# Performance work log

Hardware: AMD Instinct MI355X
Metric: run time of the kernel (lower is better)

## Reference

```python
import jax, jax.numpy as jnp
import numpy as np

B, H, S, D = 1, 16, 4096, 64
TEMPERATURE = 8.0          # sqrt(d_k)
WINDOW_SIZE = 256
HALF_WINDOW = WINDOW_SIZE // 2
NEG_INF = -1000000000.0


def setup_inputs() -> dict:
    key = jax.random.key(0)
    kq, kk, kv = jax.random.split(key, 3)
    q = jax.random.normal(kq, (B, H, S, D), dtype=jnp.float32)
    k = jax.random.normal(kk, (B, H, S, D), dtype=jnp.float32)
    v = jax.random.normal(kv, (B, H, S, D), dtype=jnp.float32)
    return {"q": q, "k": k, "v": v}


def reference(q, k, v):
    # q,k,v: [B,H,S,D]
    seq = q.shape[2]
    attn = jnp.einsum('bhqd,bhkd->bhqk', q, k) / TEMPERATURE  # [B,H,S,S]
    if seq > WINDOW_SIZE:
        idx = jnp.arange(seq)
        # torch loop: row i allows columns [i-half, i+half] inclusive
        win = jnp.abs(idx[:, None] - idx[None, :]) <= HALF_WINDOW  # [S,S]
        attn = jnp.where(win[None, None, :, :], attn, NEG_INF)
    attn = jax.nn.softmax(attn, axis=-1)  # dropout p=0 -> identity
    out = jnp.einsum('bhqk,bhkd->bhqd', attn, v)
    return (out, attn)
```

## Files before the change

kernel.cpp:

```cpp
#include <hip/hip_runtime.h>
#include <hip/hip_bf16.h>


typedef short bf16x8 __attribute__((ext_vector_type(8)));
typedef float f32x4  __attribute__((ext_vector_type(4)));
typedef unsigned int u32;
typedef unsigned short u16;

namespace {
constexpr int S = 4096, H = 16, Dh = 64, TR = 16, HW = 128, NCH = 5;
constexpr int UW  = NCH * 64;
constexpr int KP  = 72;
constexpr int PBW = UW + 8;
}

__device__ __forceinline__ u16 f2bf(float x) {
    u32 u = __float_as_uint(x);
    return (u16)((u + 0x7fffu + ((u >> 16) & 1u)) >> 16);
}
__device__ __forceinline__ float bf2f(u16 h) {
    return __uint_as_float(((u32)h) << 16);
}

__global__ __launch_bounds__(256, 4)
void wattn(const float* __restrict__ q, const float* __restrict__ k,
           const float* __restrict__ v, float* __restrict__ out,
           float* __restrict__ attn)
{
    __shared__ __align__(16) u16 hbuf[16768];
    __shared__ float red[TR * 4];
    __shared__ float inv_row[TR];
    u16* qh_ = hbuf;
    u16* ql_ = hbuf + 1152;
    u16* kh_ = hbuf + 2304;
    u16* kl_ = hbuf + 6912;
    u16* pb_ = hbuf + 11520;

    const int tid  = threadIdx.x;
    const int wave = tid >> 6, lane = tid & 63;
    const int g = lane >> 4, m = lane & 15;

    int bx = blockIdx.x;
    bx = (bx & 7) * (H * (S / TR) / 8) + (bx >> 3);
    const int h  = bx >> 8;
    const int r0 = (bx & 255) * TR;
    const int c0 = max(0, r0 - HW);
    const int c1 = min(S - 1, r0 + TR - 1 + HW);

    const float* qp = q + ((size_t)h * S + r0) * Dh;
    const float* kp = k + (size_t)h * S * Dh;
    const float* vp = v + (size_t)h * S * Dh;

    {
        const int row = tid >> 4, d4 = (tid & 15) * 4;
        float4 t = *(const float4*)(qp + row * Dh + d4);
        float xs[4] = {t.x, t.y, t.z, t.w};
        u16* dh = qh_ + row * KP + d4;
        u16* dl = ql_ + row * KP + d4;
        #pragma unroll
        for (int i = 0; i < 4; ++i) {
            u16 hi = f2bf(xs[i]);
            dh[i] = hi;
            dl[i] = f2bf(xs[i] - bf2f(hi));
        }
    }
    __syncthreads();

    bf16x8 aqh[2], aql[2];
    #pragma unroll
    for (int ks = 0; ks < 2; ++ks) {
        aqh[ks] = *(const bf16x8*)(qh_ + m * KP + ks * 32 + g * 8);
        aql[ks] = *(const bf16x8*)(ql_ + m * KP + ks * 32 + g * 8);
    }

    f32x4 sc[NCH];
    #pragma unroll
    for (int cc = 0; cc < NCH; ++cc) {
        const int col = tid >> 2, d16 = (tid & 3) * 16;
        const int cg  = min(c0 + cc * 64 + col, S - 1);
        const float* src = kp + (size_t)cg * Dh + d16;
        u16* dh = kh_ + col * KP + d16;
        u16* dl = kl_ + col * KP + d16;
        #pragma unroll
        for (int i4 = 0; i4 < 4; ++i4) {
            float4 t = *(const float4*)(src + i4 * 4);
            float xs[4] = {t.x, t.y, t.z, t.w};
            #pragma unroll
            for (int i = 0; i < 4; ++i) {
                u16 hi = f2bf(xs[i]);
                dh[i4 * 4 + i] = hi;
                dl[i4 * 4 + i] = f2bf(xs[i] - bf2f(hi));
            }
        }
        __syncthreads();
        f32x4 acc = {0.f, 0.f, 0.f, 0.f};
        #pragma unroll
        for (int ks = 0; ks < 2; ++ks) {
            bf16x8 bh = *(const bf16x8*)(kh_ + (wave * 16 + m) * KP + ks * 32 + g * 8);
            bf16x8 bl = *(const bf16x8*)(kl_ + (wave * 16 + m) * KP + ks * 32 + g * 8);
            acc = __builtin_amdgcn_mfma_f32_16x16x32_bf16(aqh[ks], bh, acc, 0, 0, 0);
            acc = __builtin_amdgcn_mfma_f32_16x16x32_bf16(aql[ks], bh, acc, 0, 0, 0);
            acc = __builtin_amdgcn_mfma_f32_16x16x32_bf16(aqh[ks], bl, acc, 0, 0, 0);
        }
        sc[cc] = acc;
        __syncthreads();
    }

    float rs[4] = {0.f, 0.f, 0.f, 0.f};
    #pragma unroll
    for (int cc = 0; cc < NCH; ++cc) {
        const int colg = c0 + cc * 64 + wave * 16 + m;
        #pragma unroll
        for (int w = 0; w < 4; ++w) {
            const int row = r0 + g * 4 + w;
            const float l = sc[cc][w] * 0.125f;
            const bool ok = (colg >= row - HW) && (colg <= row + HW) && (colg <= c1);
            const float ev = ok ? __expf(l) : 0.f;
            rs[w] += ev;
            pb_[(g * 4 + w) * PBW + cc * 64 + wave * 16 + m] = f2bf(ev);
        }
    }
    #pragma unroll
    for (int off = 1; off < 16; off <<= 1) {
        #pragma unroll
        for (int w = 0; w < 4; ++w) rs[w] += __shfl_xor(rs[w], off, 64);
    }
    if (m == 0) {
        #pragma unroll
        for (int w = 0; w < 4; ++w) red[(g * 4 + w) * 4 + wave] = rs[w];
    }
    __syncthreads();
    if (tid < TR) {
        float4 p4 = *(const float4*)(red + tid * 4);
        inv_row[tid] = 1.0f / (p4.x + p4.y + p4.z + p4.w);
    }
    __syncthreads();

    {
        float* arow = attn + ((size_t)h * S + r0) * S;
        const int c0q = c0 >> 2;
        for (int r = 0; r < TR; ++r) {
            const float inv = inv_row[r];
            float4* dst = (float4*)(arow + (size_t)r * S);
            #pragma unroll
            for (int kk = 0; kk < 4; ++kk) {
                const int c4 = tid + 256 * kk;
                const int o4 = c4 - c0q;
                float4 val = {0.f, 0.f, 0.f, 0.f};
                if ((unsigned)o4 < (unsigned)(UW / 4)) {
                    ushort4 hh = *(const ushort4*)(pb_ + r * PBW + o4 * 4);
                    val.x = bf2f(hh.x) * inv; val.y = bf2f(hh.y) * inv;
                    val.z = bf2f(hh.z) * inv; val.w = bf2f(hh.w) * inv;
                }
                dst[c4] = val;
            }
        }
    }

    f32x4 oacc = {0.f, 0.f, 0.f, 0.f};
    for (int cc = 0; cc < NCH; ++cc) {
        __syncthreads();
        const int j = tid & 63, dbase = (tid >> 6) * 16;
        const int jg = min(c0 + cc * 64 + j, S - 1);
        const float* src = vp + (size_t)jg * Dh + dbase;
        #pragma unroll
        for (int i4 = 0; i4 < 4; ++i4) {
            float4 t = *(const float4*)(src + i4 * 4);
            float xs[4] = {t.x, t.y, t.z, t.w};
            #pragma unroll
            for (int i = 0; i < 4; ++i)
                kh_[(dbase + i4 * 4 + i) * KP + j] = f2bf(xs[i]);
        }
        __syncthreads();
        #pragma unroll
        for (int ks = 0; ks < 2; ++ks) {
            bf16x8 ap = *(const bf16x8*)(pb_ + m * PBW + cc * 64 + ks * 32 + g * 8);
            bf16x8 bv = *(const bf16x8*)(kh_ + (wave * 16 + m) * KP + ks * 32 + g * 8);
            oacc = __builtin_amdgcn_mfma_f32_16x16x32_bf16(ap, bv, oacc, 0, 0, 0);
        }
    }

    float4 inv4 = *(const float4*)(inv_row + g * 4);
    float* op = out + (((size_t)h * S + r0 + g * 4) * Dh) + wave * 16 + m;
    #pragma unroll
    for (int w = 0; w < 4; ++w) {
        const float iw = (w == 0) ? inv4.x : (w == 1) ? inv4.y : (w == 2) ? inv4.z : inv4.w;
        op[(size_t)w * Dh] = oacc[w] * iw;
    }
}

extern "C" void kernel_launch(void* const* d_in, const int* in_sizes, int n_in,
                              void* d_out, int out_size, void* d_ws, size_t ws_size,
                              hipStream_t stream) {
    const float* q = (const float*)d_in[0];
    const float* k = (const float*)d_in[1];
    const float* v = (const float*)d_in[2];
    float* out  = (float*)d_out;
    float* attn = out + (size_t)H * S * Dh;
    wattn<<<dim3(H * (S / TR)), dim3(256), 0, stream>>>(q, k, v, out, attn);
}
```

Before: 1.100 ms.

## Precompute bf16 hi/lo K and transposed V in a prep kernel, drop LDS staging

```diff
diff --git a/kernel.cpp b/kernel.cpp
--- a/kernel.cpp
+++ b/kernel.cpp
@@ -10,7 +10,6 @@
 namespace {
 constexpr int S = 4096, H = 16, Dh = 64, TR = 16, HW = 128, NCH = 5;
 constexpr int UW  = NCH * 64;
-constexpr int KP  = 72;
 constexpr int PBW = UW + 8;
 }
 
@@ -22,21 +21,71 @@
     return __uint_as_float(((u32)h) << 16);
 }
 
+__global__ __launch_bounds__(256)
+void prep(const float* __restrict__ k, const float* __restrict__ v,
+          u16* __restrict__ k_hi, u16* __restrict__ k_lo, u16* __restrict__ v_t)
+{
+    __shared__ u16 vt[Dh * 65];
+    const int tid = threadIdx.x;
+    const int h  = blockIdx.x >> 6;
+    const int s0 = (blockIdx.x & 63) * 64;
+    const int r = tid >> 2, dseg = (tid & 3) * 16;
+
+    {
+        const float* src = k + ((size_t)(h * S + s0 + r) * Dh + dseg);
+        u16 hi[16] __attribute__((aligned(16)));
+        u16 lo[16] __attribute__((aligned(16)));
+        #pragma unroll
+        for (int i4 = 0; i4 < 4; ++i4) {
+            float4 t = *(const float4*)(src + i4 * 4);
+            float xs[4] = {t.x, t.y, t.z, t.w};
+            #pragma unroll
+            for (int i = 0; i < 4; ++i) {
+                u16 hh = f2bf(xs[i]);
+                hi[i4 * 4 + i] = hh;
+                lo[i4 * 4 + i] = f2bf(xs[i] - bf2f(hh));
+            }
+        }
+        const size_t o = (size_t)(h * S + s0 + r) * Dh + dseg;
+        *(int4*)(k_hi + o)     = *(const int4*)(hi);
+        *(int4*)(k_hi + o + 8) = *(const int4*)(hi + 8);
+        *(int4*)(k_lo + o)     = *(const int4*)(lo);
+        *(int4*)(k_lo + o + 8) = *(const int4*)(lo + 8);
+    }
+    {
+        const float* src = v + ((size_t)(h * S + s0 + r) * Dh + dseg);
+        #pragma unroll
+        for (int i4 = 0; i4 < 4; ++i4) {
+            float4 t = *(const float4*)(src + i4 * 4);
+            float xs[4] = {t.x, t.y, t.z, t.w};
+            #pragma unroll
+            for (int i = 0; i < 4; ++i)
+                vt[(dseg + i4 * 4 + i) * 65 + r] = f2bf(xs[i]);
+        }
+    }
+    __syncthreads();
+    {
+        const int d = tid >> 2, rseg = (tid & 3) * 16;
+        u16 tmp[16] __attribute__((aligned(16)));
+        #pragma unroll
+        for (int i = 0; i < 16; ++i) tmp[i] = vt[d * 65 + rseg + i];
+        const size_t o = (size_t)(h * Dh + d) * S + s0 + rseg;
+        *(int4*)(v_t + o)     = *(const int4*)(tmp);
+        *(int4*)(v_t + o + 8) = *(const int4*)(tmp + 8);
+    }
+}
+
 __global__ __launch_bounds__(256, 4)
-void wattn(const float* __restrict__ q, const float* __restrict__ k,
-           const float* __restrict__ v, float* __restrict__ out,
-           float* __restrict__ attn)
+void wattn(const float* __restrict__ q,
+           const u16* __restrict__ k_hi, const u16* __restrict__ k_lo,
+           const u16* __restrict__ v_t,
+           float* __restrict__ out, float* __restrict__ attn)
 {
-    __shared__ __align__(16) u16 hbuf[16768];
+    __shared__ __align__(16) u16 pb_[TR * PBW];
     __shared__ float red[TR * 4];
     __shared__ float inv_row[TR];
-    u16* qh_ = hbuf;
-    u16* ql_ = hbuf + 1152;
-    u16* kh_ = hbuf + 2304;
-    u16* kl_ = hbuf + 6912;
-    u16* pb_ = hbuf + 11520;
-
-    const int tid  = threadIdx.x;
+
+    const int tid = threadIdx.x;
     const int wave = tid >> 6, lane = tid & 63;
     const int g = lane >> 4, m = lane & 15;
 
@@ -47,63 +96,39 @@
     const int c0 = max(0, r0 - HW);
     const int c1 = min(S - 1, r0 + TR - 1 + HW);
 
-    const float* qp = q + ((size_t)h * S + r0) * Dh;
-    const float* kp = k + (size_t)h * S * Dh;
-    const float* vp = v + (size_t)h * S * Dh;
-
-    {
-        const int row = tid >> 4, d4 = (tid & 15) * 4;
-        float4 t = *(const float4*)(qp + row * Dh + d4);
-        float xs[4] = {t.x, t.y, t.z, t.w};
-        u16* dh = qh_ + row * KP + d4;
-        u16* dl = ql_ + row * KP + d4;
-        #pragma unroll
-        for (int i = 0; i < 4; ++i) {
-            u16 hi = f2bf(xs[i]);
-            dh[i] = hi;
-            dl[i] = f2bf(xs[i] - bf2f(hi));
-        }
-    }
-    __syncthreads();
-
     bf16x8 aqh[2], aql[2];
-    #pragma unroll
-    for (int ks = 0; ks < 2; ++ks) {
-        aqh[ks] = *(const bf16x8*)(qh_ + m * KP + ks * 32 + g * 8);
-        aql[ks] = *(const bf16x8*)(ql_ + m * KP + ks * 32 + g * 8);
+    {
+        const float* qrow = q + (size_t)(h * S + r0 + m) * Dh + g * 8;
+        #pragma unroll
+        for (int ks = 0; ks < 2; ++ks) {
+            float4 t0 = *(const float4*)(qrow + ks * 32);
+            float4 t1 = *(const float4*)(qrow + ks * 32 + 4);
+            float xs[8] = {t0.x, t0.y, t0.z, t0.w, t1.x, t1.y, t1.z, t1.w};
+            #pragma unroll
+            for (int i = 0; i < 8; ++i) {
+                u16 hh = f2bf(xs[i]);
+                aqh[ks][i] = (short)hh;
+                aql[ks][i] = (short)f2bf(xs[i] - bf2f(hh));
+            }
+        }
     }
 
     f32x4 sc[NCH];
     #pragma unroll
     for (int cc = 0; cc < NCH; ++cc) {
-        const int col = tid >> 2, d16 = (tid & 3) * 16;
-        const int cg  = min(c0 + cc * 64 + col, S - 1);
-        const float* src = kp + (size_t)cg * Dh + d16;
-        u16* dh = kh_ + col * KP + d16;
-        u16* dl = kl_ + col * KP + d16;
-        #pragma unroll
-        for (int i4 = 0; i4 < 4; ++i4) {
-            float4 t = *(const float4*)(src + i4 * 4);
-            float xs[4] = {t.x, t.y, t.z, t.w};
-            #pragma unroll
-            for (int i = 0; i < 4; ++i) {
-                u16 hi = f2bf(xs[i]);
-                dh[i4 * 4 + i] = hi;
-                dl[i4 * 4 + i] = f2bf(xs[i] - bf2f(hi));
-            }
-        }
-        __syncthreads();
+        const int col = min(c0 + cc * 64 + wave * 16 + m, S - 1);
+        const u16* ph = k_hi + (size_t)(h * S + col) * Dh + g * 8;
+        const u16* pl = k_lo + (size_t)(h * S + col) * Dh + g * 8;
         f32x4 acc = {0.f, 0.f, 0.f, 0.f};
         #pragma unroll
         for (int ks = 0; ks < 2; ++ks) {
-            bf16x8 bh = *(const bf16x8*)(kh_ + (wave * 16 + m) * KP + ks * 32 + g * 8);
-            bf16x8 bl = *(const bf16x8*)(kl_ + (wave * 16 + m) * KP + ks * 32 + g * 8);
+            bf16x8 bh = *(const bf16x8*)(ph + ks * 32);
+            bf16x8 bl = *(const bf16x8*)(pl + ks * 32);
             acc = __builtin_amdgcn_mfma_f32_16x16x32_bf16(aqh[ks], bh, acc, 0, 0, 0);
             acc = __builtin_amdgcn_mfma_f32_16x16x32_bf16(aql[ks], bh, acc, 0, 0, 0);
             acc = __builtin_amdgcn_mfma_f32_16x16x32_bf16(aqh[ks], bl, acc, 0, 0, 0);
         }
         sc[cc] = acc;
-        __syncthreads();
     }
 
     float rs[4] = {0.f, 0.f, 0.f, 0.f};
@@ -113,9 +138,8 @@
         #pragma unroll
         for (int w = 0; w < 4; ++w) {
             const int row = r0 + g * 4 + w;
-            const float l = sc[cc][w] * 0.125f;
             const bool ok = (colg >= row - HW) && (colg <= row + HW) && (colg <= c1);
-            const float ev = ok ? __expf(l) : 0.f;
+            const float ev = ok ? __expf(sc[cc][w] * 0.125f) : 0.f;
             rs[w] += ev;
             pb_[(g * 4 + w) * PBW + cc * 64 + wave * 16 + m] = f2bf(ev);
         }
@@ -136,8 +160,29 @@
     }
     __syncthreads();
 
-    {
-        float* arow = attn + ((size_t)h * S + r0) * S;
+    f32x4 oacc = {0.f, 0.f, 0.f, 0.f};
+    {
+        const u16* vrow = v_t + (size_t)(h * Dh + wave * 16 + m) * S;
+        #pragma unroll
+        for (int cc = 0; cc < NCH; ++cc) {
+            #pragma unroll
+            for (int ks = 0; ks < 2; ++ks) {
+                const int j = min(c0 + cc * 64 + ks * 32 + g * 8, S - 8);
+                bf16x8 ap = *(const bf16x8*)(pb_ + m * PBW + cc * 64 + ks * 32 + g * 8);
+                bf16x8 bv = *(const bf16x8*)(vrow + j);
+                oacc = __builtin_amdgcn_mfma_f32_16x16x32_bf16(ap, bv, oacc, 0, 0, 0);
+            }
+        }
+    }
+    {
+        float* op = out + (size_t)(h * S + r0 + g * 4) * Dh + wave * 16 + m;
+        #pragma unroll
+        for (int w = 0; w < 4; ++w)
+            op[(size_t)w * Dh] = oacc[w] * inv_row[g * 4 + w];
+    }
+
+    {
+        float* arow = attn + ((size_t)(h * S + r0)) * S;
         const int c0q = c0 >> 2;
         for (int r = 0; r < TR; ++r) {
             const float inv = inv_row[r];
@@ -156,37 +201,6 @@
             }
         }
     }
-
-    f32x4 oacc = {0.f, 0.f, 0.f, 0.f};
-    for (int cc = 0; cc < NCH; ++cc) {
-        __syncthreads();
-        const int j = tid & 63, dbase = (tid >> 6) * 16;
-        const int jg = min(c0 + cc * 64 + j, S - 1);
-        const float* src = vp + (size_t)jg * Dh + dbase;
-        #pragma unroll
-        for (int i4 = 0; i4 < 4; ++i4) {
-            float4 t = *(const float4*)(src + i4 * 4);
-            float xs[4] = {t.x, t.y, t.z, t.w};
-            #pragma unroll
-            for (int i = 0; i < 4; ++i)
-                kh_[(dbase + i4 * 4 + i) * KP + j] = f2bf(xs[i]);
-        }
-        __syncthreads();
-        #pragma unroll
-        for (int ks = 0; ks < 2; ++ks) {
-            bf16x8 ap = *(const bf16x8*)(pb_ + m * PBW + cc * 64 + ks * 32 + g * 8);
-            bf16x8 bv = *(const bf16x8*)(kh_ + (wave * 16 + m) * KP + ks * 32 + g * 8);
-            oacc = __builtin_amdgcn_mfma_f32_16x16x32_bf16(ap, bv, oacc, 0, 0, 0);
-        }
-    }
-
-    float4 inv4 = *(const float4*)(inv_row + g * 4);
-    float* op = out + (((size_t)h * S + r0 + g * 4) * Dh) + wave * 16 + m;
-    #pragma unroll
-    for (int w = 0; w < 4; ++w) {
-        const float iw = (w == 0) ? inv4.x : (w == 1) ? inv4.y : (w == 2) ? inv4.z : inv4.w;
-        op[(size_t)w * Dh] = oacc[w] * iw;
-    }
 }
 
 extern "C" void kernel_launch(void* const* d_in, const int* in_sizes, int n_in,
@@ -197,5 +211,9 @@
     const float* v = (const float*)d_in[2];
     float* out  = (float*)d_out;
     float* attn = out + (size_t)H * S * Dh;
-    wattn<<<dim3(H * (S / TR)), dim3(256), 0, stream>>>(q, k, v, out, attn);
-}
+    u16* k_hi = (u16*)d_ws;
+    u16* k_lo = k_hi + (size_t)H * S * Dh;
+    u16* v_t  = k_lo + (size_t)H * S * Dh;
+    prep <<<dim3(H * (S / 64)), dim3(256), 0, stream>>>(k, v, k_hi, k_lo, v_t);
+    wattn<<<dim3(H * (S / TR)), dim3(256), 0, stream>>>(q, k_hi, k_lo, v_t, out, attn);
+}
```

Measured after the change: 1.107 ms. About the same (+0.7%).
